# Optimization experiments

Measured on AMD Instinct MI355X. Metric: run time of the kernel, lower is better.

## Reference

```python
import math
import jax, jax.numpy as jnp
import numpy as np

WQ = (24, 24)  # query window size
WK = (12, 12)  # key window size
NH = 8         # heads
D = 256        # d_model


def _ln(x, g, b, eps=1e-5):
    m = x.mean(-1, keepdims=True)
    v = ((x - m) ** 2).mean(-1, keepdims=True)
    return (x - m) / jnp.sqrt(v + eps) * g + b


def _sine_pos(F, Hp, Wp):
    # Faithful to PositionEmbeddingSine(normalize=True) applied to an NHWC tensor:
    # dim F (grid height) plays the role of channels; returns (F, Hp, Wp).
    npf = F // 2
    scale = 2.0 * math.pi
    eps = 1e-5
    y = jnp.arange(1, Hp + 1, dtype=jnp.float32) / (Hp + eps) * scale
    x = jnp.arange(1, Wp + 1, dtype=jnp.float32) / (Wp + eps) * scale
    dim_t = 10000.0 ** (2.0 * (jnp.arange(npf) // 2).astype(jnp.float32) / npf)
    def enc(e):
        p = e[:, None] / dim_t
        return jnp.stack([jnp.sin(p[:, 0::2]), jnp.cos(p[:, 1::2])], axis=2).reshape(e.shape[0], npf)
    py = enc(y)  # (Hp, npf)
    px = enc(x)  # (Wp, npf)
    pos = jnp.concatenate([
        jnp.broadcast_to(py[:, None, :], (Hp, Wp, npf)),
        jnp.broadcast_to(px[None, :, :], (Hp, Wp, npf))], axis=-1)
    return pos.transpose(2, 0, 1)


def _interp_ac(x, Ho, Wo):
    # bilinear, align_corners=True; x: (B, C, H, W)
    B, C, H, W = x.shape
    ys = jnp.linspace(0.0, H - 1.0, Ho)
    xs = jnp.linspace(0.0, W - 1.0, Wo)
    y0 = jnp.floor(ys).astype(jnp.int32); y1 = jnp.minimum(y0 + 1, H - 1); wy = ys - y0
    x0 = jnp.floor(xs).astype(jnp.int32); x1 = jnp.minimum(x0 + 1, W - 1); wx = xs - x0
    rows = x[:, :, y0, :] * (1 - wy)[None, None, :, None] + x[:, :, y1, :] * wy[None, None, :, None]
    return rows[:, :, :, x0] * (1 - wx) + rows[:, :, :, x1] * wx


def _wpart(x, wh, ww):
    B, H, W, C = x.shape
    return x.reshape(B, H // wh, wh, W // ww, ww, C).transpose(0, 1, 3, 2, 4, 5).reshape(-1, wh * ww, C)


def _avgpool(x, wh, ww):
    B, H, W, C = x.shape
    return x.reshape(B, H // wh, wh, W // ww, ww, C).mean(axis=(2, 4))


def _forward(x1, x2, q_w, q_b, k_w, k_b, v_w, v_b, q2_w, q2_b, k2_w, k2_b, v2_w, v2_b,
             proj_w, proj_b, proj_g, proj_beta, n1_g, n1_b, n2_g, n2_b,
             fc1_w, fc1_b, fc2_w, fc2_b):
    B, C1, H1, W1 = x1.shape
    _, C2, H2, W2 = x2.shape
    hd = D // NH
    x1n = x1.transpose(0, 2, 3, 1)
    sc = _ln(x1n @ proj_w + proj_b, proj_g, proj_beta)
    sc = _interp_ac(sc.transpose(0, 3, 1, 2), H2, W2).transpose(0, 2, 3, 1)
    x1p = jnp.pad(x1n, ((0, 0), (0, (-H1) % WK[0]), (0, (-W1) % WK[1]), (0, 0)))
    x2n = x2.transpose(0, 2, 3, 1)
    x2p = jnp.pad(x2n, ((0, 0), (0, (-H2) % WQ[0]), (0, (-W2) % WQ[1]), (0, 0)))
    H2p, W2p = x2p.shape[1], x2p.shape[2]
    qw = _wpart(x2p, *WQ)  # (B*nw, 576, C2)
    kw = _wpart(x1p, *WK)  # (B*nw, 144, C1)
    Bn, N1, _ = qw.shape
    def heads(t):
        return t.reshape(t.shape[0], t.shape[1], NH, hd).transpose(0, 2, 1, 3)
    q = heads(qw @ q_w + q_b)
    k = heads(kw @ k_w + k_b)
    v = heads(kw @ v_w + v_b)
    # NOTE: faithful to the source: scale = head_dim**(-0.0) == 1.0 and NO softmax here
    attn = q @ k.transpose(0, 1, 3, 2)
    o = (attn @ v).transpose(0, 2, 1, 3).reshape(Bn, N1, D)
    nwh, nww = H2p // WQ[0], W2p // WQ[1]
    o = o.reshape(B, nwh, nww, WQ[0], WQ[1], D).transpose(0, 1, 3, 2, 4, 5).reshape(B, H2p, W2p, D)
    qf = x2p + o
    # global (pooled) cross-attention branch
    qg = _avgpool(x2p, *WQ)
    qg = qg + _sine_pos(qg.shape[1], qg.shape[2], qg.shape[3])[None]
    kg = _avgpool(x1p, *WK)
    kg = kg + _sine_pos(kg.shape[1], kg.shape[2], kg.shape[3])[None]
    qg = qg.reshape(B, -1, C2)
    kg = kg.reshape(B, -1, C1)
    Nw = qg.shape[1]
    qg2 = heads(qg @ q2_w + q2_b)
    kg2 = heads(kg @ k2_w + k2_b)
    vg = heads(kg @ v2_w + v2_b)
    a2 = jax.nn.softmax(qg2 @ kg2.transpose(0, 1, 3, 2), axis=-1)
    og = (a2 @ vg).transpose(0, 2, 1, 3).reshape(B, Nw, D)
    og = og.transpose(0, 2, 1).reshape(B, D, nwh, nww)
    og = _interp_ac(og, H2p, W2p).transpose(0, 2, 3, 1)
    qf = (qf + og)[:, :H2, :W2, :]
    h = _ln(qf, n1_g, n1_b)
    h = jax.nn.gelu(h @ fc1_w + fc1_b, approximate=False) @ fc2_w + fc2_b
    out = sc + h
    return _ln(out, n2_g, n2_b).transpose(0, 3, 1, 2)


def setup_inputs() -> dict:
    key = jax.random.key(0)
    ks = jax.random.split(key, 12)
    B, C1, C2 = 2, 512, 256
    H1, W1, H2, W2 = 96, 96, 192, 192
    s = 0.02
    def lin(k, i, o):
        return jax.random.normal(k, (i, o), jnp.float32) * s
    return {
        'x1': jax.random.normal(ks[0], (B, C1, H1, W1), jnp.float32),
        'x2': jax.random.normal(ks[1], (B, C2, H2, W2), jnp.float32),
        'q_w': lin(ks[2], C2, D), 'q_b': jnp.zeros((D,), jnp.float32),
        'k_w': lin(ks[3], C1, D), 'k_b': jnp.zeros((D,), jnp.float32),
        'v_w': lin(ks[4], C1, D), 'v_b': jnp.zeros((D,), jnp.float32),
        'q2_w': lin(ks[5], C2, D), 'q2_b': jnp.zeros((D,), jnp.float32),
        'k2_w': lin(ks[6], C1, D), 'k2_b': jnp.zeros((D,), jnp.float32),
        'v2_w': lin(ks[7], C1, D), 'v2_b': jnp.zeros((D,), jnp.float32),
        'proj_w': lin(ks[8], C1, D), 'proj_b': jnp.zeros((D,), jnp.float32),
        'proj_g': jnp.ones((D,), jnp.float32), 'proj_beta': jnp.zeros((D,), jnp.float32),
        'n1_g': jnp.ones((D,), jnp.float32), 'n1_b': jnp.zeros((D,), jnp.float32),
        'n2_g': jnp.ones((D,), jnp.float32), 'n2_b': jnp.zeros((D,), jnp.float32),
        'fc1_w': lin(ks[9], D, 2 * D), 'fc1_b': jnp.zeros((2 * D,), jnp.float32),
        'fc2_w': lin(ks[10], 2 * D, D), 'fc2_b': jnp.zeros((D,), jnp.float32),
    }


def reference(x1, x2, q_w, q_b, k_w, k_b, v_w, v_b, q2_w, q2_b, k2_w, k2_b, v2_w, v2_b,
              proj_w, proj_b, proj_g, proj_beta, n1_g, n1_b, n2_g, n2_b,
              fc1_w, fc1_b, fc2_w, fc2_b):
    return _forward(x1, x2, q_w, q_b, k_w, k_b, v_w, v_b, q2_w, q2_b, k2_w, k2_b, v2_w, v2_b,
                    proj_w, proj_b, proj_g, proj_beta, n1_g, n1_b, n2_g, n2_b,
                    fc1_w, fc1_b, fc2_w, fc2_b)
```

## Files before the change

### kernel.cpp

```cpp
#include <hip/hip_runtime.h>
#include <math.h>


#define HW1 9216L
#define HW2 36864L
#define M1  18432L
#define M2  73728L

typedef __attribute__((ext_vector_type(8))) short short8;
typedef __attribute__((ext_vector_type(4))) float f32x4;
typedef unsigned short u16;

__device__ __forceinline__ short f2bf(float f)
{
    unsigned u = __builtin_bit_cast(unsigned, f);
    u = (u + 0x7fff + ((u >> 16) & 1)) >> 16;
    return (short)u;
}
__device__ __forceinline__ float bf2f(u16 u)
{
    unsigned x = ((unsigned)u) << 16;
    return __builtin_bit_cast(float, x);
}
__device__ __forceinline__ float gelu_exact(float v)
{
    return 0.5f * v * (1.0f + erff(v * 0.70710678118654752f));
}

__global__ __launch_bounds__(256) void wcvt(
    const float* __restrict__ pw, const float* __restrict__ kw,
    const float* __restrict__ vw, const float* __restrict__ qw,
    const float* __restrict__ f1, const float* __restrict__ f2,
    const float* __restrict__ kb, const float* __restrict__ vb,
    u16* __restrict__ pwT, u16* __restrict__ kwT, u16* __restrict__ vwT,
    u16* __restrict__ f1T, u16* __restrict__ f2T,
    u16* __restrict__ qwN, float* __restrict__ kvb)
{
    int bx = blockIdx.x, t = threadIdx.x;
    if (bx >= 176) {
        kvb[t] = kb[t];
        kvb[256 + t] = vb[t];
        return;
    }
    if (bx >= 160) {
        int k0 = (bx - 160) * 16;
#pragma unroll
        for (int kk = 0; kk < 16; ++kk)
            qwN[(long)(k0 + kk) * 256 + t] = (u16)f2bf(qw[(long)(k0 + kk) * 256 + t]);
        return;
    }
    const float* src; u16* dst; int K, ldN = 256, kt, n0 = 0;
    if (bx < 32)       { src = pw; dst = pwT; K = 512; kt = bx; }
    else if (bx < 64)  { src = kw; dst = kwT; K = 512; kt = bx - 32; }
    else if (bx < 96)  { src = vw; dst = vwT; K = 512; kt = bx - 64; }
    else if (bx < 128) { int j = bx - 96; src = f1; dst = f1T; K = 256;
                         ldN = 512; kt = j >> 1; n0 = (j & 1) * 256; }
    else               { src = f2; dst = f2T; K = 512; kt = bx - 128; }
    int n = n0 + t, k0 = kt * 16;
    short s[16];
#pragma unroll
    for (int kk = 0; kk < 16; ++kk) s[kk] = f2bf(src[(long)(k0 + kk) * ldN + n]);
    *(short8*)&dst[(long)n * K + k0]     = *(short8*)&s[0];
    *(short8*)&dst[(long)n * K + k0 + 8] = *(short8*)&s[8];
}

__device__ __forceinline__ float pe4(int t, float e)
{
    if (t == 0) return sinf(e);
    if (t == 1) return cosf(e);
    if (t == 2) return sinf(e * 0.01f);
    return cosf(e * 0.01f);
}

__global__ __launch_bounds__(256) void x1t(
    const float* __restrict__ x1, u16* __restrict__ x1bf, float* __restrict__ kg)
{
    __shared__ short T[6144];
    __shared__ float rw[64][8];
    const int blk = blockIdx.x;
    const int b = blk / 768, rem = blk % 768;
    const int cg = rem / 96, y = rem % 96;
    const int t = threadIdx.x;

    ((float2*)rw)[t] = float2{0.f, 0.f};
    __syncthreads();

    const float* src = x1 + ((long)(b * 512 + cg * 64)) * HW1 + (long)y * 96;
#pragma unroll
    for (int k = 0; k < 6; ++k) {
        int idx = t + k * 256;
        int c = idx / 24, col4 = idx % 24;
        float4 v = *(const float4*)(src + (long)c * HW1 + col4 * 4);
        atomicAdd(&rw[c][col4 / 3], v.x + v.y + v.z + v.w);
        int chh = c >> 1, cb = c & 1;
        const float* vf = (const float*)&v;
#pragma unroll
        for (int j = 0; j < 4; ++j) {
            int pix = col4 * 4 + j;
            int word = pix * 32 + (chh ^ (((pix >> 2) & 7) << 2));
            T[word * 2 + cb] = f2bf(vf[j]);
        }
    }
    __syncthreads();
    u16* dst = x1bf + ((long)b * HW1 + (long)y * 96) * 512 + cg * 64;
#pragma unroll
    for (int k = 0; k < 3; ++k) {
        int idx = t + k * 256;
        int pix = idx >> 3, j = idx & 7;
        int w0 = pix * 32 + ((j * 4) ^ (((pix >> 2) & 7) << 2));
        *(short8*)(dst + (long)pix * 512 + j * 8) = *(short8*)&T[w0 * 2];
    }

    {
        int wy = y / 12;
#pragma unroll
        for (int u = 0; u < 2; ++u) {
            int cell = t * 2 + u;
            int c = cell >> 3, wx = cell & 7;
            atomicAdd(kg + (long)(b * 64 + wy * 8 + wx) * 512 + cg * 64 + c,
                      rw[c][wx] * (1.0f / 144.0f));
        }
    }
    if (y % 12 == 0) {
        const float TWO_PI = 6.283185307179586f;
        int wy = y / 12;
#pragma unroll
        for (int u = 0; u < 2; ++u) {
            int cell = t * 2 + u;
            int gxx = cell & 7, c = cg * 64 + (cell >> 3);
            float pos;
            if (wy < 4) pos = pe4(wy,     (gxx + 1) * (TWO_PI / (8.0f + 1e-5f)));
            else        pos = pe4(wy - 4, (c + 1)   * (TWO_PI / (512.0f + 1e-5f)));
            atomicAdd(kg + (long)(b * 64 + wy * 8 + gxx) * 512 + c, pos);
        }
    }
}

__global__ __launch_bounds__(256) void x2t(
    const float* __restrict__ x2, u16* __restrict__ x2pm, float* __restrict__ qg)
{
    __shared__ short T[12288];
    __shared__ float qsum[64][8];
    const int blk = blockIdx.x;
    const int b = blk / 768, rem = blk % 768;
    const int cg = rem / 192, h = rem % 192;
    const int t = threadIdx.x;

    ((float2*)qsum)[t] = float2{0.f, 0.f};
    __syncthreads();

    const float* src = x2 + ((long)(b * 256 + cg * 64) * 192 + h) * 192;
#pragma unroll
    for (int k = 0; k < 12; ++k) {
        int idx = t + k * 256;
        int c = idx / 48, col4 = idx % 48;
        float4 v = *(const float4*)(src + (long)c * HW2 + col4 * 4);
        atomicAdd(&qsum[c][col4 / 6], v.x + v.y + v.z + v.w);
        int chh = c >> 1, cb = c & 1;
        const float* vf = (const float*)&v;
#pragma unroll
        for (int j = 0; j < 4; ++j) {
            int pix = col4 * 4 + j;
            int word = pix * 32 + (chh ^ (((pix >> 2) & 7) << 2));
            T[word * 2 + cb] = f2bf(vf[j]);
        }
    }
    __syncthreads();

    u16* dst = x2pm + ((long)b * HW2 + (long)h * 192) * 256 + cg * 64;
#pragma unroll
    for (int k = 0; k < 6; ++k) {
        int idx = t + k * 256;
        int pix = idx >> 3, j = idx & 7;
        int w0 = pix * 32 + ((j * 4) ^ (((pix >> 2) & 7) << 2));
        *(short8*)(dst + (long)pix * 256 + j * 8) = *(short8*)&T[w0 * 2];
    }

    {
        int wy = h / 24;
#pragma unroll
        for (int u = 0; u < 2; ++u) {
            int cell = t * 2 + u;
            int c = cell >> 3, wx = cell & 7;
            atomicAdd(qg + (long)(b * 64 + wy * 8 + wx) * 256 + cg * 64 + c,
                      qsum[c][wx] * (1.0f / 576.0f));
        }
    }
    if (h % 24 == 0) {
        const float TWO_PI = 6.283185307179586f;
        int wy = h / 24;
#pragma unroll
        for (int u = 0; u < 2; ++u) {
            int cell = t * 2 + u;
            int gxx = cell & 7, c = cg * 64 + (cell >> 3);
            float pos;
            if (wy < 4) pos = pe4(wy,     (gxx + 1) * (TWO_PI / (8.0f + 1e-5f)));
            else        pos = pe4(wy - 4, (c + 1)   * (TWO_PI / (256.0f + 1e-5f)));
            atomicAdd(qg + (long)(b * 64 + wy * 8 + gxx) * 256 + c, pos);
        }
    }
}

__global__ __launch_bounds__(256) void proj_ln(
    const u16* __restrict__ A, const u16* __restrict__ BT,
    const float* __restrict__ bias, const float* __restrict__ g,
    const float* __restrict__ beta, u16* __restrict__ Cout)
{
    __shared__ short pool[64 * 72 + 256 * 72];
    short* As = pool;
    short* Bs = pool + 64 * 72;
    const int t = threadIdx.x;
    const long m0 = (long)blockIdx.x * 64;
    const int w = t >> 6, lane = t & 63;
    const int lm = lane & 15, lq = lane >> 4;

    f32x4 acc[16] = {};
    for (int k0 = 0; k0 < 512; k0 += 64) {
#pragma unroll
        for (int it = 0; it < 2; ++it) {
            int idx = t + it * 256;
            int r = idx >> 3, q = idx & 7;
            *(short8*)&As[r * 72 + q * 8] = *(const short8*)(A + (m0 + r) * 512 + k0 + q * 8);
        }
#pragma unroll
        for (int it = 0; it < 8; ++it) {
            int idx = t + it * 256;
            int n = idx >> 3, q = idx & 7;
            *(short8*)&Bs[n * 72 + q * 8] = *(const short8*)(BT + (long)n * 512 + k0 + q * 8);
        }
        __syncthreads();
#pragma unroll
        for (int kk = 0; kk < 64; kk += 32) {
            short8 af = *(short8*)&As[(w * 16 + lm) * 72 + kk + lq * 8];
#pragma unroll
            for (int c = 0; c < 16; ++c) {
                short8 bf = *(short8*)&Bs[(c * 16 + lm) * 72 + kk + lq * 8];
                acc[c] = __builtin_amdgcn_mfma_f32_16x16x32_bf16(af, bf, acc[c], 0, 0, 0);
            }
        }
        __syncthreads();
    }
#pragma unroll
    for (int c = 0; c < 16; ++c) {
        float bv = bias[c * 16 + lm];
#pragma unroll
        for (int i = 0; i < 4; ++i) acc[c][i] += bv;
    }
    short* ob = pool;
#pragma unroll
    for (int i = 0; i < 4; ++i) {
        float s = 0.f, s2 = 0.f;
#pragma unroll
        for (int c = 0; c < 16; ++c) { float v = acc[c][i]; s += v; s2 += v * v; }
#pragma unroll
        for (int o = 8; o > 0; o >>= 1) {
            s  += __shfl_xor(s,  o, 64);
            s2 += __shfl_xor(s2, o, 64);
        }
        float mean = s * (1.0f / 256.0f);
        float var  = s2 * (1.0f / 256.0f) - mean * mean;
        float rs   = rsqrtf(var + 1e-5f);
        int row = w * 16 + lq * 4 + i;
#pragma unroll
        for (int c = 0; c < 16; ++c) {
            int col = c * 16 + lm;
            ob[row * 264 + col] = f2bf((acc[c][i] - mean) * rs * g[col] + beta[col]);
        }
    }
    __syncthreads();
    {
        int sr = t >> 2, q4 = (t & 3) * 64;
        u16* Cp = Cout + (m0 + sr) * 256 + q4;
#pragma unroll
        for (int q = 0; q < 8; ++q)
            *(short8*)(Cp + q * 8) = *(short8*)&ob[sr * 264 + q4 + q * 8];
    }
}

template<int EPI>
__global__ __launch_bounds__(256) void gemm_lds(
    const u16* __restrict__ A, const u16* __restrict__ BT,
    const float* __restrict__ bias, u16* __restrict__ C,
    int N, int K, int ldA)
{
    __shared__ short pool[18432];
    short* As = pool;
    short* Bs = pool + 128 * 72;
    const int tid = threadIdx.x;
    const int m0 = blockIdx.y * 128;
    const int n0 = blockIdx.x * 128;
    const int w = tid >> 6, lane = tid & 63;
    const int wm = (w & 1) * 64, wn = (w >> 1) * 64;
    const int lm = lane & 15, lq = lane >> 4;

    const int sr = tid >> 1, sh = (tid & 1) * 32;
    const u16* Ap = A  + (long)(m0 + sr) * ldA + sh;
    const u16* Bp = BT + (long)(n0 + sr) * K   + sh;

    f32x4 acc[4][4] = {};

    for (int k0 = 0; k0 < K; k0 += 64) {
#pragma unroll
        for (int q = 0; q < 4; ++q)
            *(short8*)&As[sr * 72 + sh + q * 8] = *(const short8*)(Ap + k0 + q * 8);
#pragma unroll
        for (int q = 0; q < 4; ++q)
            *(short8*)&Bs[sr * 72 + sh + q * 8] = *(const short8*)(Bp + k0 + q * 8);
        __syncthreads();
#pragma unroll
        for (int kk = 0; kk < 64; kk += 32) {
            short8 af[4], bfr[4];
#pragma unroll
            for (int r = 0; r < 4; ++r) af[r]  = *(short8*)&As[(wm + r * 16 + lm) * 72 + kk + lq * 8];
#pragma unroll
            for (int c = 0; c < 4; ++c) bfr[c] = *(short8*)&Bs[(wn + c * 16 + lm) * 72 + kk + lq * 8];
#pragma unroll
            for (int r = 0; r < 4; ++r)
#pragma unroll
                for (int c = 0; c < 4; ++c)
                    acc[r][c] = __builtin_amdgcn_mfma_f32_16x16x32_bf16(af[r], bfr[c], acc[r][c], 0, 0, 0);
        }
        __syncthreads();
    }

    short* ob = pool;
#pragma unroll
    for (int r = 0; r < 4; ++r)
#pragma unroll
        for (int i = 0; i < 4; ++i) {
            int row = wm + r * 16 + lq * 4 + i;
#pragma unroll
            for (int c = 0; c < 4; ++c) {
                int jl = wn + c * 16 + lm;
                float v = acc[r][c][i] + bias[n0 + jl];
                if (EPI == 1) v = gelu_exact(v);
                ob[row * 136 + jl] = f2bf(v);
            }
        }
    __syncthreads();
    int m = tid >> 1, half = (tid & 1) * 64;
    u16* Cp = C + (long)(m0 + m) * N + n0 + half;
#pragma unroll
    for (int q = 0; q < 8; ++q)
        *(short8*)(Cp + q * 8) = *(short8*)&ob[m * 136 + half + q * 8];
}

__global__ __launch_bounds__(64) void ktv_w(
    const u16* __restrict__ kv16, const u16* __restrict__ qwN,
    const float* __restrict__ qb, u16* __restrict__ wT, float* __restrict__ bias_w)
{
    __shared__ short pool[10368 + 1280];
    short* kt  = pool;
    short* vt  = pool + 5184;
    short* kt2 = pool + 10368;
    short* wout = pool;

    const int blk = blockIdx.x;
    const int win = blk >> 3, hd = blk & 7;
    const int b = win >> 6, wy = (win >> 3) & 7, wx = win & 7;
    const int t = threadIdx.x;
    const int lm = t & 15, lq = t >> 4;

    {
        int c = t >> 1, p0 = 144 + (t & 1) * 8;
#pragma unroll
        for (int j = 0; j < 8; ++j) {
            kt[c * 162 + p0 + j] = 0;
            vt[c * 162 + p0 + j] = 0;
        }
    }
    const int pq = t >> 2, c8 = (t & 3) * 8;
#pragma unroll
    for (int it = 0; it < 9; ++it) {
        int p = it * 16 + pq;
        int py = p / 12, px = p % 12;
        long m = (long)b * HW1 + (long)(wy * 12 + py) * 96 + wx * 12 + px;
        short8 kvk = *(const short8*)(kv16 + m * 512 + hd * 32 + c8);
        short8 kvv = *(const short8*)(kv16 + m * 512 + 256 + hd * 32 + c8);
#pragma unroll
        for (int j = 0; j < 8; ++j) {
            kt[(c8 + j) * 162 + p] = kvk[j];
            vt[(c8 + j) * 162 + p] = kvv[j];
        }
    }
    __syncthreads();
    f32x4 acc[2][2] = {};
#pragma unroll
    for (int kk = 0; kk < 160; kk += 32) {
        short8 af[2], bf[2];
#pragma unroll
        for (int r = 0; r < 2; ++r) af[r] = *(short8*)&kt[(r * 16 + lm) * 162 + kk + lq * 8];
#pragma unroll
        for (int c = 0; c < 2; ++c) bf[c] = *(short8*)&vt[(c * 16 + lm) * 162 + kk + lq * 8];
#pragma unroll
        for (int r = 0; r < 2; ++r)
#pragma unroll
            for (int c = 0; c < 2; ++c)
                acc[r][c] = __builtin_amdgcn_mfma_f32_16x16x32_bf16(af[r], bf[c], acc[r][c], 0, 0, 0);
    }
#pragma unroll
    for (int r = 0; r < 2; ++r)
#pragma unroll
        for (int c = 0; c < 2; ++c)
#pragma unroll
            for (int i = 0; i < 4; ++i)
                kt2[(c * 16 + lm) * 40 + r * 16 + lq * 4 + i] = f2bf(acc[r][c][i]);
    __syncthreads();
    if (t < 32) {
        float s = 0.f;
#pragma unroll
        for (int tt = 0; tt < 32; ++tt)
            s += bf2f((u16)kt2[t * 40 + tt]) * qb[hd * 32 + tt];
        bias_w[(long)blk * 32 + t] = s;
    }
    short8 af2[2];
#pragma unroll
    for (int r = 0; r < 2; ++r) af2[r] = *(short8*)&kt2[(r * 16 + lm) * 40 + lq * 8];
#pragma unroll
    for (int nt = 0; nt < 16; ++nt) {
        short8 bf = *(const short8*)(qwN + (long)(nt * 16 + lm) * 256 + hd * 32 + lq * 8);
        f32x4 a2[2] = {};
#pragma unroll
        for (int r = 0; r < 2; ++r)
            a2[r] = __builtin_amdgcn_mfma_f32_16x16x32_bf16(af2[r], bf, a2[r], 0, 0, 0);
#pragma unroll
        for (int r = 0; r < 2; ++r)
#pragma unroll
            for (int i = 0; i < 4; ++i)
                wout[(r * 16 + lq * 4 + i) * 264 + nt * 16 + lm] = f2bf(a2[r][i]);
    }
    __syncthreads();
    {
        int row = t >> 1, half = (t & 1) * 128;
        u16* dst = wT + ((long)blk * 32 + row) * 256 + half;
#pragma unroll
        for (int q = 0; q < 16; ++q)
            *(short8*)(dst + q * 8) = *(short8*)&wout[row * 264 + half + q * 8];
    }
}

__global__ __launch_bounds__(256) void wattn_ln3(
    const u16* __restrict__ x2pm, const u16* __restrict__ wT,
    const float* __restrict__ bias_w, const float* __restrict__ og,
    u16* __restrict__ hln, const float* __restrict__ n1g,
    const float* __restrict__ n1b)
{
    __shared__ short qs[48 * 288];

    const int t = threadIdx.x;
    const int blk = blockIdx.x;
    const int strip = blk % 12, win = blk / 12;
    const int b = win >> 6, wy = (win >> 3) & 7, wxw = win & 7;
    const int hh0 = wy * 24 + strip * 2;
    const int w = t >> 6, lane = t & 63;
    const int lm = lane & 15, lq = lane >> 4;

    long pbase[3];
#pragma unroll
    for (int r = 0; r < 3; ++r) {
        int p = r * 16 + lm;
        pbase[r] = ((long)b * HW2 + (long)(hh0 + p / 24) * 192 + wxw * 24 + (p % 24)) * 256;
    }
    const u16* wbase = wT + (long)win * 256 * 256;

    f32x4 acc[3][4] = {};
#pragma unroll 2
    for (int kc = 0; kc < 8; ++kc) {
        const int ko = kc * 32 + lq * 8;
        short8 af[3], bfr[4];
#pragma unroll
        for (int r = 0; r < 3; ++r)
            af[r] = *(const short8*)(x2pm + pbase[r] + ko);
#pragma unroll
        for (int c = 0; c < 4; ++c)
            bfr[c] = *(const short8*)(wbase + (long)(w * 64 + c * 16 + lm) * 256 + ko);
#pragma unroll
        for (int r = 0; r < 3; ++r)
#pragma unroll
            for (int c = 0; c < 4; ++c)
                acc[r][c] = __builtin_amdgcn_mfma_f32_16x16x32_bf16(af[r], bfr[c], acc[r][c], 0, 0, 0);
    }

#pragma unroll
    for (int c = 0; c < 4; ++c) {
        float bv = bias_w[(long)win * 256 + w * 64 + c * 16 + lm];
#pragma unroll
        for (int r = 0; r < 3; ++r)
#pragma unroll
            for (int i = 0; i < 4; ++i) {
                int p = r * 16 + lq * 4 + i;
                int col = w * 64 + c * 16 + lm;
                qs[p * 288 + (col ^ (((p >> 2) & 3) << 4))] = f2bf(acc[r][c][i] + bv);
            }
    }
    __syncthreads();

    float4 g4 = *(const float4*)(n1g + lane * 4);
    float4 b4 = *(const float4*)(n1b + lane * 4);
    const float* ogb0 = og + (long)b * 64 * 256;
#pragma unroll
    for (int pp = 0; pp < 12; ++pp) {
        int p = w * 12 + pp;
        int hh = hh0 + (p / 24), ww = wxw * 24 + (p % 24);
        float fy = hh * (7.0f / 191.0f);
        int y0 = (int)fy; int y1 = min(y0 + 1, 7); float wyf = fy - y0;
        float fx = ww * (7.0f / 191.0f);
        int x0 = (int)fx; int x1 = min(x0 + 1, 7); float wxf = fx - x0;
        float w00 = (1.f - wyf) * (1.f - wxf), w01 = (1.f - wyf) * wxf;
        float w10 = wyf * (1.f - wxf),         w11 = wyf * wxf;
        float4 q00 = *(const float4*)(ogb0 + (y0 * 8 + x0) * 256 + lane * 4);
        float4 q01 = *(const float4*)(ogb0 + (y0 * 8 + x1) * 256 + lane * 4);
        float4 q10 = *(const float4*)(ogb0 + (y1 * 8 + x0) * 256 + lane * 4);
        float4 q11 = *(const float4*)(ogb0 + (y1 * 8 + x1) * 256 + lane * 4);
        long pix = (long)b * HW2 + (long)hh * 192 + ww;
        ushort4 rv = *(const ushort4*)(x2pm + pix * 256 + lane * 4);
        int sw = ((p >> 2) & 3) << 4;
        ushort4 ov = *(ushort4*)&qs[p * 288 + ((lane * 4) ^ sw)];
        float xv0 = bf2f(rv.x) + bf2f(ov.x) + (w00 * q00.x + w01 * q01.x + w10 * q10.x + w11 * q11.x);
        float xv1 = bf2f(rv.y) + bf2f(ov.y) + (w00 * q00.y + w01 * q01.y + w10 * q10.y + w11 * q11.y);
        float xv2 = bf2f(rv.z) + bf2f(ov.z) + (w00 * q00.z + w01 * q01.z + w10 * q10.z + w11 * q11.z);
        float xv3 = bf2f(rv.w) + bf2f(ov.w) + (w00 * q00.w + w01 * q01.w + w10 * q10.w + w11 * q11.w);
        float s  = xv0 + xv1 + xv2 + xv3;
        float s2 = xv0 * xv0 + xv1 * xv1 + xv2 * xv2 + xv3 * xv3;
#pragma unroll
        for (int o = 32; o > 0; o >>= 1) {
            s  += __shfl_xor(s,  o, 64);
            s2 += __shfl_xor(s2, o, 64);
        }
        float mean = s * (1.0f / 256.0f);
        float var  = s2 * (1.0f / 256.0f) - mean * mean;
        float rs   = rsqrtf(var + 1e-5f);
        ushort4 o4;
        o4.x = (u16)f2bf((xv0 - mean) * rs * g4.x + b4.x);
        o4.y = (u16)f2bf((xv1 - mean) * rs * g4.y + b4.y);
        o4.z = (u16)f2bf((xv2 - mean) * rs * g4.z + b4.z);
        o4.w = (u16)f2bf((xv3 - mean) * rs * g4.w + b4.w);
        *(ushort4*)(hln + pix * 256 + lane * 4) = o4;
    }
}

__global__ __launch_bounds__(256) void gemm64m(
    const float* __restrict__ qg, const float* __restrict__ kg,
    const float* __restrict__ q2w, const float* __restrict__ q2b,
    const float* __restrict__ k2w, const float* __restrict__ k2b,
    const float* __restrict__ v2w, const float* __restrict__ v2b,
    float* __restrict__ qg2, float* __restrict__ kg2, float* __restrict__ vgb)
{
    const float* A; const float* Bm; const float* bias; float* C; int K, ldA;
    int z = blockIdx.z;
    if (z == 0)      { A = qg; Bm = q2w; bias = q2b; C = qg2; K = 256; ldA = 256; }
    else if (z == 1) { A = kg; Bm = k2w; bias = k2b; C = kg2; K = 512; ldA = 512; }
    else             { A = kg; Bm = v2w; bias = v2b; C = vgb; K = 512; ldA = 512; }
    const int N = 256;
    constexpr int BK = 16;
    __shared__ float As[BK][68];
    __shared__ float Bs[BK][68];
    const int tid = threadIdx.x;
    const int m0 = blockIdx.y * 64;
    const int n0 = blockIdx.x * 64;
    const int tm = (tid >> 4) << 2;
    const int tn = (tid & 15) << 2;
    float acc[4][4] = {};
    for (int k0 = 0; k0 < K; k0 += BK) {
#pragma unroll
        for (int it = 0; it < 4; ++it) {
            int idx = tid + it * 256;
            int my = idx >> 4, kx = idx & 15;
            As[kx][my] = A[(long)(m0 + my) * ldA + (k0 + kx)];
        }
#pragma unroll
        for (int it = 0; it < 4; ++it) {
            int idx = tid + it * 256;
            int ky = idx >> 6, nx = idx & 63;
            Bs[ky][nx] = Bm[(long)(k0 + ky) * N + (n0 + nx)];
        }
        __syncthreads();
#pragma unroll
        for (int kk = 0; kk < BK; ++kk) {
            float a[4], b[4];
#pragma unroll
            for (int i = 0; i < 4; ++i) a[i] = As[kk][tm + i];
#pragma unroll
            for (int j = 0; j < 4; ++j) b[j] = Bs[kk][tn + j];
#pragma unroll
            for (int i = 0; i < 4; ++i)
#pragma unroll
                for (int j = 0; j < 4; ++j) acc[i][j] += a[i] * b[j];
        }
        __syncthreads();
    }
#pragma unroll
    for (int i = 0; i < 4; ++i) {
        long row = (long)(m0 + tm + i) * N;
#pragma unroll
        for (int j = 0; j < 4; ++j)
            C[row + n0 + tn + j] = acc[i][j] + bias[n0 + tn + j];
    }
}

__global__ __launch_bounds__(256) void gattn(
    const float* __restrict__ qg2, const float* __restrict__ kg2,
    const float* __restrict__ vg, float* __restrict__ og)
{
    __shared__ float qh[64][33], kh[64][33], vh[64][33];
    __shared__ float S[64][65];
    __shared__ float rinv[64];
    int blk = blockIdx.x;
    int b = blk >> 3, hd = blk & 7;
    int t = threadIdx.x;
#pragma unroll
    for (int it = 0; it < 8; ++it) {
        int idx = t + it * 256;
        int n = idx >> 5, i = idx & 31;
        long src = (long)(b * 64 + n) * 256 + hd * 32 + i;
        qh[n][i] = qg2[src];
        kh[n][i] = kg2[src];
        vh[n][i] = vg[src];
    }
    __syncthreads();
    int r = t >> 2, qq = t & 3, c0 = qq * 16;
    for (int c = c0; c < c0 + 16; ++c) {
        float s = 0.f;
#pragma unroll
        for (int i = 0; i < 32; ++i) s += qh[r][i] * kh[c][i];
        S[r][c] = s;
    }
    __syncthreads();
    float mx = -1e30f;
    for (int c = c0; c < c0 + 16; ++c) mx = fmaxf(mx, S[r][c]);
    mx = fmaxf(mx, __shfl_xor(mx, 1, 64));
    mx = fmaxf(mx, __shfl_xor(mx, 2, 64));
    float sm = 0.f;
    for (int c = c0; c < c0 + 16; ++c) {
        float e = expf(S[r][c] - mx);
        S[r][c] = e;
        sm += e;
    }
    sm += __shfl_xor(sm, 1, 64);
    sm += __shfl_xor(sm, 2, 64);
    if (qq == 0) rinv[r] = 1.0f / sm;
    __syncthreads();
    int n = t >> 2, j0 = (t & 3) * 8;
    float inv = rinv[n];
    for (int j = j0; j < j0 + 8; ++j) {
        float s = 0.f;
        for (int c = 0; c < 64; ++c) s += S[n][c] * vh[c][j];
        og[(long)(b * 64 + n) * 256 + hd * 32 + j] = s * inv;
    }
}

__global__ __launch_bounds__(256) void final_k3(
    const u16* __restrict__ mlp, const u16* __restrict__ sc,
    const float* __restrict__ g, const float* __restrict__ bb,
    float* __restrict__ out)
{
    __shared__ float lnb[32][258];
    int blk = blockIdx.x;
    int b = blk / 1152;
    int rem = blk - b * 1152;
    int hh = rem / 6, ww0 = (rem % 6) * 32;
    int wv = threadIdx.x >> 6, lane = threadIdx.x & 63;
    int c0 = lane * 4;
    float4 g4 = *(const float4*)(g + c0);
    float4 b4 = *(const float4*)(bb + c0);
    float fy = hh * (95.0f / 191.0f);
    int y0 = (int)fy; int y1 = min(y0 + 1, 95); float wy = fy - y0;
    const u16* scb = sc + (long)b * 9216 * 256 + c0;
#pragma unroll
    for (int i = 0; i < 8; ++i) {
        int p = wv * 8 + i;
        int ww = ww0 + p;
        float fx = ww * (95.0f / 191.0f);
        int x0 = (int)fx; int x1 = min(x0 + 1, 95); float wx = fx - x0;
        ushort4 u00 = *(const ushort4*)(scb + (long)(y0 * 96 + x0) * 256);
        ushort4 u01 = *(const ushort4*)(scb + (long)(y0 * 96 + x1) * 256);
        ushort4 u10 = *(const ushort4*)(scb + (long)(y1 * 96 + x0) * 256);
        ushort4 u11 = *(const ushort4*)(scb + (long)(y1 * 96 + x1) * 256);
        long m = ((long)b * 192 + hh) * 192 + ww;
        ushort4 um = *(const ushort4*)(mlp + m * 256 + c0);
        float w00 = (1.f - wy) * (1.f - wx), w01 = (1.f - wy) * wx;
        float w10 = wy * (1.f - wx),         w11 = wy * wx;
        float xv0 = bf2f(um.x) + w00 * bf2f(u00.x) + w01 * bf2f(u01.x) + w10 * bf2f(u10.x) + w11 * bf2f(u11.x);
        float xv1 = bf2f(um.y) + w00 * bf2f(u00.y) + w01 * bf2f(u01.y) + w10 * bf2f(u10.y) + w11 * bf2f(u11.y);
        float xv2 = bf2f(um.z) + w00 * bf2f(u00.z) + w01 * bf2f(u01.z) + w10 * bf2f(u10.z) + w11 * bf2f(u11.z);
        float xv3 = bf2f(um.w) + w00 * bf2f(u00.w) + w01 * bf2f(u01.w) + w10 * bf2f(u10.w) + w11 * bf2f(u11.w);
        float s  = xv0 + xv1 + xv2 + xv3;
        float s2 = xv0 * xv0 + xv1 * xv1 + xv2 * xv2 + xv3 * xv3;
#pragma unroll
        for (int o = 32; o > 0; o >>= 1) {
            s  += __shfl_xor(s,  o, 64);
            s2 += __shfl_xor(s2, o, 64);
        }
        float mean = s * (1.0f / 256.0f);
        float var  = s2 * (1.0f / 256.0f) - mean * mean;
        float rs   = rsqrtf(var + 1e-5f);
        lnb[p][c0 + 0] = (xv0 - mean) * rs * g4.x + b4.x;
        lnb[p][c0 + 1] = (xv1 - mean) * rs * g4.y + b4.y;
        lnb[p][c0 + 2] = (xv2 - mean) * rs * g4.z + b4.z;
        lnb[p][c0 + 3] = (xv3 - mean) * rs * g4.w + b4.w;
    }
    __syncthreads();
    int tw = threadIdx.x & 31, cg = threadIdx.x >> 5;
#pragma unroll
    for (int cc = 0; cc < 32; ++cc) {
        int c = cg * 32 + cc;
        out[((long)(b * 256 + c) * 192 + hh) * 192 + ww0 + tw] = lnb[tw][c];
    }
}

extern "C" void kernel_launch(void* const* d_in, const int* in_sizes, int n_in,
                              void* d_out, int out_size, void* d_ws, size_t ws_size,
                              hipStream_t stream)
{
    const float* x1     = (const float*)d_in[0];
    const float* x2     = (const float*)d_in[1];
    const float* q_w    = (const float*)d_in[2];
    const float* q_b    = (const float*)d_in[3];
    const float* k_w    = (const float*)d_in[4];
    const float* k_b    = (const float*)d_in[5];
    const float* v_w    = (const float*)d_in[6];
    const float* v_b    = (const float*)d_in[7];
    const float* q2_w   = (const float*)d_in[8];
    const float* q2_b   = (const float*)d_in[9];
    const float* k2_w   = (const float*)d_in[10];
    const float* k2_b   = (const float*)d_in[11];
    const float* v2_w   = (const float*)d_in[12];
    const float* v2_b   = (const float*)d_in[13];
    const float* proj_w = (const float*)d_in[14];
    const float* proj_b = (const float*)d_in[15];
    const float* proj_g = (const float*)d_in[16];
    const float* proj_bt= (const float*)d_in[17];
    const float* n1_g   = (const float*)d_in[18];
    const float* n1_b   = (const float*)d_in[19];
    const float* n2_g   = (const float*)d_in[20];
    const float* n2_b   = (const float*)d_in[21];
    const float* fc1_w  = (const float*)d_in[22];
    const float* fc1_b  = (const float*)d_in[23];
    const float* fc2_w  = (const float*)d_in[24];
    const float* fc2_b  = (const float*)d_in[25];
    float* out = (float*)d_out;

    char* p = (char*)d_ws;
    u16*   scb  = (u16*)p;    p += M1 * 256 * 2;
    u16*   pwT  = (u16*)p;    p += 262144;
    u16*   kwT  = (u16*)p;    p += 262144;
    u16*   vwT  = (u16*)p;    p += 262144;
    u16*   f1T  = (u16*)p;    p += 262144;
    u16*   f2T  = (u16*)p;    p += 262144;
    u16*   qwN  = (u16*)p;    p += 131072;
    float* kvb  = (float*)p;  p += 2048;
    float* bias_w = (float*)p; p += 131072;
    u16*   wT   = (u16*)p;    p += 1024L * 32 * 256 * 2;
    u16*   kv16 = (u16*)p;    p += M1 * 512 * 2;
    u16*   hln  = (u16*)p;    p += M2 * 256 * 2;
    u16*   h1c  = (u16*)p;    p += 36864L * 512 * 2;
    u16*   mlpb = (u16*)p;    p += M2 * 256 * 2;
    float* qg   = (float*)p;  p += 128L * 256 * 4;
    float* kg   = (float*)p;  p += 128L * 512 * 4;
    float* qg2  = (float*)p;  p += 128L * 256 * 4;
    float* kg2  = (float*)p;  p += 128L * 256 * 4;
    float* vgb  = (float*)p;  p += 128L * 256 * 4;
    float* ogb  = (float*)p;  p += 128L * 256 * 4;

    u16* x2pm = mlpb;
    u16* x1bf = hln;

    dim3 blk(256);

    hipMemsetAsync(qg, 0, (128L * 256 + 128L * 512) * 4, stream);

    wcvt<<<dim3(177), blk, 0, stream>>>(proj_w, k_w, v_w, q_w, fc1_w, fc2_w,
                                        k_b, v_b, pwT, kwT, vwT, f1T, f2T,
                                        qwN, kvb);
    x1t<<<dim3(1536), blk, 0, stream>>>(x1, x1bf, kg);
    x2t<<<dim3(1536), blk, 0, stream>>>(x2, x2pm, qg);

    proj_ln<<<dim3(288), blk, 0, stream>>>(x1bf, pwT, proj_b, proj_g, proj_bt, scb);

    gemm_lds<0><<<dim3(4, 144), blk, 0, stream>>>(x1bf, kwT, kvb, kv16, 512, 512, 512);

    ktv_w<<<dim3(1024), dim3(64), 0, stream>>>(kv16, qwN, q_b, wT, bias_w);

    gemm64m<<<dim3(4, 2, 3), blk, 0, stream>>>(qg, kg, q2_w, q2_b, k2_w, k2_b,
                                               v2_w, v2_b, qg2, kg2, vgb);
    gattn<<<dim3(16), blk, 0, stream>>>(qg2, kg2, vgb, ogb);

    wattn_ln3<<<dim3(1536), blk, 0, stream>>>(x2pm, wT, bias_w, ogb, hln, n1_g, n1_b);

    for (int c2 = 0; c2 < 2; ++c2) {
        const u16* aoff = hln  + (long)c2 * 36864 * 256;
        u16*       coff = mlpb + (long)c2 * 36864 * 256;
        gemm_lds<1><<<dim3(4, 288), blk, 0, stream>>>(aoff, f1T, fc1_b, h1c, 512, 256, 256);
        gemm_lds<0><<<dim3(2, 288), blk, 0, stream>>>(h1c, f2T, fc2_b, coff, 256, 512, 512);
    }

    final_k3<<<dim3(2304), blk, 0, stream>>>(mlpb, scb, n2_g, n2_b, out);
}
```

Before: 566.7 us.

## Use direct global-to-LDS loads with XOR swizzle and XCD-aware block remap

```diff
diff --git a/kernel.cpp b/kernel.cpp
--- a/kernel.cpp
+++ b/kernel.cpp
@@ -10,6 +10,9 @@
 typedef __attribute__((ext_vector_type(8))) short short8;
 typedef __attribute__((ext_vector_type(4))) float f32x4;
 typedef unsigned short u16;
+
+#define AS1 __attribute__((address_space(1)))
+#define AS3 __attribute__((address_space(3)))
 
 __device__ __forceinline__ short f2bf(float f)
 {
@@ -281,39 +284,50 @@
 __global__ __launch_bounds__(256) void gemm_lds(
     const u16* __restrict__ A, const u16* __restrict__ BT,
     const float* __restrict__ bias, u16* __restrict__ C,
-    int N, int K, int ldA)
-{
-    __shared__ short pool[18432];
+    int N, int K, int ldA, int ny)
+{
+    __shared__ short pool[17408];
     short* As = pool;
-    short* Bs = pool + 128 * 72;
+    short* Bs = pool + 8192;
     const int tid = threadIdx.x;
-    const int m0 = blockIdx.y * 128;
-    const int n0 = blockIdx.x * 128;
+    const int blk = blockIdx.x, G = gridDim.x, per = G >> 3;
+    const int Lid = (blk & 7) * per + (blk >> 3);
+    const int nx = G / ny;
+    const int m0 = (Lid / nx) * 128;
+    const int n0 = (Lid % nx) * 128;
     const int w = tid >> 6, lane = tid & 63;
     const int wm = (w & 1) * 64, wn = (w >> 1) * 64;
     const int lm = lane & 15, lq = lane >> 4;
 
-    const int sr = tid >> 1, sh = (tid & 1) * 32;
-    const u16* Ap = A  + (long)(m0 + sr) * ldA + sh;
-    const u16* Bp = BT + (long)(n0 + sr) * K   + sh;
+    const int srow = w * 32 + (lane >> 3);
+    const int scs  = ((lane & 7) * 8) ^ ((lane >> 3) << 3);
+    const u16* Ap = A  + (long)(m0 + srow) * ldA + scs;
+    const u16* Bp = BT + (long)(n0 + srow) * K   + scs;
+    const int rsw = (lm & 7) << 3;
 
     f32x4 acc[4][4] = {};
 
     for (int k0 = 0; k0 < K; k0 += 64) {
 #pragma unroll
-        for (int q = 0; q < 4; ++q)
-            *(short8*)&As[sr * 72 + sh + q * 8] = *(const short8*)(Ap + k0 + q * 8);
-#pragma unroll
-        for (int q = 0; q < 4; ++q)
-            *(short8*)&Bs[sr * 72 + sh + q * 8] = *(const short8*)(Bp + k0 + q * 8);
+        for (int i = 0; i < 4; ++i)
+            __builtin_amdgcn_global_load_lds(
+                (AS1 const void*)(Ap + (long)i * 8 * ldA + k0),
+                (AS3 void*)&As[(w * 32 + i * 8) * 64], 16, 0, 0);
+#pragma unroll
+        for (int i = 0; i < 4; ++i)
+            __builtin_amdgcn_global_load_lds(
+                (AS1 const void*)(Bp + (long)i * 8 * K + k0),
+                (AS3 void*)&Bs[(w * 32 + i * 8) * 64], 16, 0, 0);
         __syncthreads();
 #pragma unroll
         for (int kk = 0; kk < 64; kk += 32) {
             short8 af[4], bfr[4];
 #pragma unroll
-            for (int r = 0; r < 4; ++r) af[r]  = *(short8*)&As[(wm + r * 16 + lm) * 72 + kk + lq * 8];
-#pragma unroll
-            for (int c = 0; c < 4; ++c) bfr[c] = *(short8*)&Bs[(wn + c * 16 + lm) * 72 + kk + lq * 8];
+            for (int r = 0; r < 4; ++r)
+                af[r]  = *(short8*)&As[(wm + r * 16 + lm) * 64 + ((kk + lq * 8) ^ rsw)];
+#pragma unroll
+            for (int c = 0; c < 4; ++c)
+                bfr[c] = *(short8*)&Bs[(wn + c * 16 + lm) * 64 + ((kk + lq * 8) ^ rsw)];
 #pragma unroll
             for (int r = 0; r < 4; ++r)
 #pragma unroll
@@ -449,7 +463,8 @@
 
     const int t = threadIdx.x;
     const int blk = blockIdx.x;
-    const int strip = blk % 12, win = blk / 12;
+    const int Lid = (blk & 7) * 192 + (blk >> 3);
+    const int strip = Lid % 12, win = Lid / 12;
     const int b = win >> 6, wy = (win >> 3) & 7, wxw = win & 7;
     const int hh0 = wy * 24 + strip * 2;
     const int w = t >> 6, lane = t & 63;
@@ -777,7 +792,7 @@
 
     proj_ln<<<dim3(288), blk, 0, stream>>>(x1bf, pwT, proj_b, proj_g, proj_bt, scb);
 
-    gemm_lds<0><<<dim3(4, 144), blk, 0, stream>>>(x1bf, kwT, kvb, kv16, 512, 512, 512);
+    gemm_lds<0><<<dim3(576), blk, 0, stream>>>(x1bf, kwT, kvb, kv16, 512, 512, 512, 144);
 
     ktv_w<<<dim3(1024), dim3(64), 0, stream>>>(kv16, qwN, q_b, wT, bias_w);
 
@@ -790,8 +805,8 @@
     for (int c2 = 0; c2 < 2; ++c2) {
         const u16* aoff = hln  + (long)c2 * 36864 * 256;
         u16*       coff = mlpb + (long)c2 * 36864 * 256;
-        gemm_lds<1><<<dim3(4, 288), blk, 0, stream>>>(aoff, f1T, fc1_b, h1c, 512, 256, 256);
-        gemm_lds<0><<<dim3(2, 288), blk, 0, stream>>>(h1c, f2T, fc2_b, coff, 256, 512, 512);
+        gemm_lds<1><<<dim3(1152), blk, 0, stream>>>(aoff, f1T, fc1_b, h1c, 512, 256, 256, 288);
+        gemm_lds<0><<<dim3(576), blk, 0, stream>>>(h1c, f2T, fc2_b, coff, 256, 512, 512, 288);
     }
 
     final_k3<<<dim3(2304), blk, 0, stream>>>(mlpb, scb, n2_g, n2_b, out);
```

New measurement: 561.7 us. Within noise of the previous version (-0.9%).
